# Kernel optimization log

Measured on AMD Instinct MI355X. Metric: run time of the kernel, lower is better.

The kernel has to match this reference:

```python
import jax, jax.numpy as jnp
import numpy as np

# Model constants (match init_kwargs / lucidrains reformer defaults where noted)
DEPTH = 2
HEADS = 8
DIM = 1024
DH = DIM // HEADS        # dim per head = 128
T = 4096                 # sequence length
BUCKET = 64              # bucket_size
NB = T // BUCKET         # n_buckets = 64
NH = 4                   # n_hashes (lucidrains default 8; reduced for memory)
B = 2                    # batch
FF_MULT = 4


def layer_norm(x, g, b):
    mu = jnp.mean(x, axis=-1, keepdims=True)
    var = jnp.mean(jnp.square(x - mu), axis=-1, keepdims=True)
    return (x - mu) * jax.lax.rsqrt(var + 1e-5) * g + b


def lsh_attn_head(qk, v, rot):
    """Single-head LSH attention. qk, v: [T, DH]; rot: [DH, NH, NB//2]."""
    t, d = qk.shape
    # --- LSH bucketing: random rotations, argmax over [rot, -rot] ---
    rotated = jnp.einsum('td,dhr->htr', qk, rot)            # [NH, T, NB//2]
    rotated = jnp.concatenate([rotated, -rotated], axis=-1)  # [NH, T, NB]
    buckets = jnp.argmax(rotated, axis=-1)                   # [NH, T]
    buckets = buckets + jnp.arange(NH)[:, None] * NB         # offset per hash round
    buckets = buckets.reshape(-1)                            # [NH*T]
    ticker = jnp.arange(NH * t)
    # stable sort by (bucket, position)
    sort_key = buckets * t + (ticker % t)
    sticker = jnp.argsort(sort_key)                          # sorted -> original flat idx
    undo = jnp.argsort(sticker)                              # original flat idx -> sorted pos
    st = sticker % t                                         # original seq positions, sorted
    sqk = qk[st]                                             # [NH*T, DH]
    sv = v[st]
    # --- chunked attention: each chunk attends to itself + previous chunk ---
    nc = NH * NB
    bq = sqk.reshape(nc, BUCKET, d)
    bv = sv.reshape(nc, BUCKET, d)
    bt = st.reshape(nc, BUCKET)
    bk = bq / jnp.sqrt(jnp.sum(bq * bq, axis=-1, keepdims=True) + 1e-12)  # unit-length keys
    look = lambda z: jnp.concatenate([z, jnp.roll(z, 1, axis=0)], axis=1)
    bk, bv2, bkt = look(bk), look(bv), look(bt)
    dots = jnp.einsum('cid,cjd->cij', bq, bk) * (d ** -0.5)  # [nc, BUCKET, 2*BUCKET]
    # self-attention mask (token attends to itself only as a last resort)
    dots = jnp.where(bt[:, :, None] == bkt[:, None, :], dots - 1e5, dots)
    lse = jax.scipy.special.logsumexp(dots, axis=-1, keepdims=True)
    probs = jnp.exp(dots - lse)
    bo = jnp.einsum('cij,cjd->cid', probs, bv2)              # [nc, BUCKET, DH]
    # --- unsort and combine hash rounds by softmax over round logsumexps ---
    o = bo.reshape(-1, d)[undo].reshape(NH, t, d)
    logits = lse.reshape(-1)[undo].reshape(NH, t, 1)
    w = jnp.exp(logits - jax.scipy.special.logsumexp(logits, axis=0, keepdims=True))
    return jnp.sum(o * w, axis=0)                            # [T, DH]


def lsh_self_attention(h, Wqk, Wv, Wo, bo, rot):
    bsz, t, _ = h.shape
    split = lambda z: z.reshape(bsz, t, HEADS, DH).transpose(0, 2, 1, 3).reshape(bsz * HEADS, t, DH)
    qk = split(h @ Wqk)
    v = split(h @ Wv)
    out = jax.vmap(lsh_attn_head, in_axes=(0, 0, None))(qk, v, rot)
    out = out.reshape(bsz, HEADS, t, DH).transpose(0, 2, 1, 3).reshape(bsz, t, HEADS * DH)
    return out @ Wo + bo


def setup_inputs() -> dict:
    key = jax.random.key(0)
    ks = jax.random.split(key, 16)
    s = 0.02
    inp = {
        'x': jax.random.normal(ks[0], (B, T, DIM), dtype=jnp.float32),
        'mask': jnp.ones((B, T), dtype=bool),
        'ln1_g': jnp.ones((DEPTH, DIM), jnp.float32),
        'ln1_b': jnp.zeros((DEPTH, DIM), jnp.float32),
        'Wqk': jax.random.normal(ks[1], (DEPTH, DIM, HEADS * DH), jnp.float32) * s,
        'Wv': jax.random.normal(ks[2], (DEPTH, DIM, HEADS * DH), jnp.float32) * s,
        'Wo': jax.random.normal(ks[3], (DEPTH, HEADS * DH, DIM), jnp.float32) * s,
        'bo': jnp.zeros((DEPTH, DIM), jnp.float32),
        'ln2_g': jnp.ones((DEPTH, DIM), jnp.float32),
        'ln2_b': jnp.zeros((DEPTH, DIM), jnp.float32),
        'W1': jax.random.normal(ks[4], (DEPTH, DIM, FF_MULT * DIM), jnp.float32) * s,
        'b1': jnp.zeros((DEPTH, FF_MULT * DIM), jnp.float32),
        'W2': jax.random.normal(ks[5], (DEPTH, FF_MULT * DIM, DIM), jnp.float32) * s,
        'b2': jnp.zeros((DEPTH, DIM), jnp.float32),
        'rot': jax.random.normal(ks[6], (DEPTH, DH, NH, NB // 2), jnp.float32),
    }
    return inp


def reference(x, mask, ln1_g, ln1_b, Wqk, Wv, Wo, bo, ln2_g, ln2_b, W1, b1, W2, b2, rot):
    # Reversible sequence: duplicate stream, f = PreNorm(LSHSelfAttention), g = PreNorm(FF)
    x1, x2 = x, x
    for l in range(DEPTH):
        a = lsh_self_attention(layer_norm(x2, ln1_g[l], ln1_b[l]),
                               Wqk[l], Wv[l], Wo[l], bo[l], rot[l])
        y1 = x1 + a
        h = layer_norm(y1, ln2_g[l], ln2_b[l])
        f = jax.nn.gelu(h @ W1[l] + b1[l]) @ W2[l] + b2[l]
        y2 = x2 + f
        x1, x2 = y1, y2
    return (x1 + x2) * 0.5
```

## Files before the change

kernel.cpp:

```cpp
#include <hip/hip_runtime.h>
#include <hip/hip_bf16.h>

#define TSEQ   4096
#define DIMM   1024
#define NHEADS 8
#define DH     128
#define NHASH  4
#define NBUCK  64
#define NCHUNK 256
#define BSZ    2
#define NBH    16
#define FFD    4096

typedef __attribute__((ext_vector_type(4))) float f32x4;
typedef __attribute__((ext_vector_type(8))) short s16x8;
typedef __attribute__((ext_vector_type(4))) short s16x4;
typedef __attribute__((ext_vector_type(2))) double f64x2;

__device__ __forceinline__ unsigned short f2bf(float f) {
    union { float f; unsigned int u; } x; x.f = f;
    unsigned int r = x.u + 0x7FFFu + ((x.u >> 16) & 1u);
    return (unsigned short)(r >> 16);
}

__device__ __forceinline__ void async16(const void* g, void* l) {
    __builtin_amdgcn_global_load_lds(
        (const __attribute__((address_space(1))) unsigned int*)g,
        (__attribute__((address_space(3))) unsigned int*)l, 16, 0, 0);
}

__device__ __forceinline__ float gelu_tanh(float x) {
    float x3 = x * x * x;
    float inner = 0.7978845608028654f * (x + 0.044715f * x3);
    return 0.5f * x * (1.0f + tanhf(inner));
}

__global__ void init_kernel(const float* __restrict__ x, float* __restrict__ X1,
                            float* __restrict__ X2, int n) {
    int i = blockIdx.x * blockDim.x + threadIdx.x;
    if (i < n) { float v = x[i]; X1[i] = v; X2[i] = v; }
}

__global__ void zero_kernel(float* __restrict__ p, int n) {
    int i = blockIdx.x * blockDim.x + threadIdx.x;
    if (i < n) p[i] = 0.f;
}

__global__ void initmw_kernel(float* __restrict__ M, float* __restrict__ W, int n) {
    int i = blockIdx.x * blockDim.x + threadIdx.x;
    if (i < n) { M[i] = -3.0e38f; W[i] = 0.f; }
}

__global__ void div_kernel(const float* __restrict__ U, const float* __restrict__ Wst,
                           unsigned short* __restrict__ AOb, int n) {
    int i = blockIdx.x * blockDim.x + threadIdx.x;
    if (i < n) {
        int row = i >> 10, col = i & 1023;
        int b = row >> 12, t = row & 4095, head = col >> 7;
        float w = Wst[(size_t)(b * 8 + head) * TSEQ + t];
        AOb[i] = f2bf(U[i] / w);
    }
}

__global__ __launch_bounds__(256) void convT_kernel(const float* __restrict__ in,
                                                    unsigned short* __restrict__ out,
                                                    int K, int N) {
    __shared__ float tile[32][33];
    int n0 = blockIdx.x * 32, k0 = blockIdx.y * 32;
    int tx = threadIdx.x & 31, ty = threadIdx.x >> 5;
    #pragma unroll
    for (int r = 0; r < 4; r++)
        tile[ty + r * 8][tx] = in[(size_t)(k0 + ty + r * 8) * N + n0 + tx];
    __syncthreads();
    #pragma unroll
    for (int r = 0; r < 4; r++)
        out[(size_t)(n0 + ty + r * 8) * K + k0 + tx] = f2bf(tile[tx][ty + r * 8]);
}

__global__ __launch_bounds__(256) void ln_bf16_kernel(const float* __restrict__ in,
                                                      const float* __restrict__ g,
                                                      const float* __restrict__ bb,
                                                      unsigned short* __restrict__ out) {
    int row = blockIdx.x;
    int tid = threadIdx.x;
    const float* xr = in + (size_t)row * DIMM;
    float v[4];
    float s = 0.f, sq = 0.f;
    #pragma unroll
    for (int k = 0; k < 4; k++) { float t = xr[tid + 256 * k]; v[k] = t; s += t; sq += t * t; }
    __shared__ float rs[256], rq[256];
    rs[tid] = s; rq[tid] = sq; __syncthreads();
    for (int off = 128; off > 0; off >>= 1) {
        if (tid < off) { rs[tid] += rs[tid + off]; rq[tid] += rq[tid + off]; }
        __syncthreads();
    }
    float mu  = rs[0] * (1.f / DIMM);
    float var = rq[0] * (1.f / DIMM) - mu * mu;
    float rstd = rsqrtf(var + 1e-5f);
    unsigned short* orow = out + (size_t)row * DIMM;
    #pragma unroll
    for (int k = 0; k < 4; k++) {
        int c = tid + 256 * k;
        orow[c] = f2bf((v[k] - mu) * rstd * g[c] + bb[c]);
    }
}

template<int OUT_BF16>
__global__ __launch_bounds__(256) void mgemm_kernel(const unsigned short* __restrict__ A,
                                                    const unsigned short* __restrict__ Bt,
                                                    const float* __restrict__ bias,
                                                    const float* __restrict__ resid,
                                                    void* __restrict__ Cv,
                                                    int M, int N, int K, int flags) {
    __shared__ __align__(16) unsigned short sA[128 * 32];
    __shared__ __align__(16) unsigned short sB[128 * 32];
    int tid = threadIdx.x;
    int wave = tid >> 6, lane = tid & 63;
    int n0 = blockIdx.x * 128, m0 = blockIdx.y * 128;
    int wr = (wave >> 1) * 64, wc = (wave & 1) * 64;
    f32x4 acc[4][4] = {};
    int c1 = tid, c2 = tid + 256;
    const unsigned short* gA1 = A + (size_t)(m0 + (c1 >> 2)) * K + (c1 & 3) * 8;
    const unsigned short* gA2 = A + (size_t)(m0 + (c2 >> 2)) * K + (c2 & 3) * 8;
    const unsigned short* gB1 = Bt + (size_t)(n0 + (c1 >> 2)) * K + (c1 & 3) * 8;
    const unsigned short* gB2 = Bt + (size_t)(n0 + (c2 >> 2)) * K + (c2 & 3) * 8;
    unsigned short* lA1 = sA + wave * 512;
    unsigned short* lA2 = sA + 2048 + wave * 512;
    unsigned short* lB1 = sB + wave * 512;
    unsigned short* lB2 = sB + 2048 + wave * 512;
    int qk8 = (lane >> 4) * 8;
    int r16 = lane & 15;
    for (int k0 = 0; k0 < K; k0 += 32) {
        __syncthreads();
        async16(gA1 + k0, lA1);
        async16(gA2 + k0, lA2);
        async16(gB1 + k0, lB1);
        async16(gB2 + k0, lB2);
        __syncthreads();
        s16x8 af[4], bf[4];
        #pragma unroll
        for (int i = 0; i < 4; i++) {
            af[i] = *(const s16x8*)&sA[(wr + i * 16 + r16) * 32 + qk8];
            bf[i] = *(const s16x8*)&sB[(wc + i * 16 + r16) * 32 + qk8];
        }
        #pragma unroll
        for (int mi = 0; mi < 4; mi++)
            #pragma unroll
            for (int ni = 0; ni < 4; ni++)
                acc[mi][ni] = __builtin_amdgcn_mfma_f32_16x16x32_bf16(af[mi], bf[ni], acc[mi][ni], 0, 0, 0);
    }
    #pragma unroll
    for (int mi = 0; mi < 4; mi++) {
        #pragma unroll
        for (int r = 0; r < 4; r++) {
            int row = m0 + wr + mi * 16 + (lane >> 4) * 4 + r;
            #pragma unroll
            for (int ni = 0; ni < 4; ni++) {
                int col = n0 + wc + ni * 16 + (lane & 15);
                float v = acc[mi][ni][r];
                if (flags & 1) v += bias[col];
                if (flags & 2) v = gelu_tanh(v);
                if (flags & 4) v += resid[(size_t)row * N + col];
                if (OUT_BF16) ((unsigned short*)Cv)[(size_t)row * N + col] = f2bf(v);
                else          ((float*)Cv)[(size_t)row * N + col] = v;
            }
        }
    }
}


__global__ __launch_bounds__(256) void ln64_kernel(const float* __restrict__ X,
                                                   const float* __restrict__ g,
                                                   const float* __restrict__ bb,
                                                   double* __restrict__ H64) {
    int row = blockIdx.x;
    int tid = threadIdx.x;
    const float* xr = X + (size_t)row * DIMM;
    __shared__ double rs[256], rq[256];
    double v[4];
    double s = 0.0, sq = 0.0;
    #pragma unroll
    for (int q = 0; q < 4; q++) {
        double t = (double)xr[tid + 256 * q];
        v[q] = t; s += t; sq += t * t;
    }
    rs[tid] = s; rq[tid] = sq; __syncthreads();
    for (int off = 128; off > 0; off >>= 1) {
        if (tid < off) { rs[tid] += rs[tid + off]; rq[tid] += rq[tid + off]; }
        __syncthreads();
    }
    double mu   = rs[0] * (1.0 / DIMM);
    double var  = rq[0] * (1.0 / DIMM) - mu * mu;
    double rstd = 1.0 / sqrt(var + 1e-5);
    double* orow = H64 + (size_t)row * DIMM;
    #pragma unroll
    for (int q = 0; q < 4; q++) {
        int c = tid + 256 * q;
        orow[c] = (v[q] - mu) * rstd * (double)g[c] + (double)bb[c];
    }
}

__global__ __launch_bounds__(256) void rcomb_kernel(const float* __restrict__ Wqk,
                                                    const float* __restrict__ rot,
                                                    double* __restrict__ R) {
    int k = blockIdx.x;
    int c0 = threadIdx.x * 4;
    int hd = c0 >> 7;
    int cc = c0 & 127;
    const float* wrow = Wqk + (size_t)k * DIMM + hd * 128;
    double a0 = 0.0, a1 = 0.0, a2 = 0.0, a3 = 0.0;
    for (int d = 0; d < 128; d++) {
        double w = (double)wrow[d];
        f32x4 r4 = *(const f32x4*)&rot[d * 128 + cc];
        a0 += w * (double)r4.x; a1 += w * (double)r4.y;
        a2 += w * (double)r4.z; a3 += w * (double)r4.w;
    }
    double* orow = R + (size_t)k * DIMM + c0;
    orow[0] = a0; orow[1] = a1; orow[2] = a2; orow[3] = a3;
}

#define RKS 16
__global__ __launch_bounds__(256, 2) void rotgemm_kernel(const double* __restrict__ H64,
                                                         const double* __restrict__ R,
                                                         int* __restrict__ bucket) {
    __shared__ double sA[RKS][130];
    __shared__ double sB[RKS][130];
    int tid = threadIdx.x;
    int tx = tid & 15, ty = tid >> 4;
    int n0 = blockIdx.x * 128, m0 = blockIdx.y * 128;
    double acc[8][8] = {};

    int arow = tid >> 1, ak = (tid & 1) * 8;
    const double* gA = H64 + (size_t)(m0 + arow) * DIMM + ak;
    int bkk = tid >> 4, bn = (tid & 15) * 8;
    const double* gB = R + (size_t)bkk * DIMM + n0 + bn;

    f64x2 a2[4], b2[4];
    #pragma unroll
    for (int u = 0; u < 4; u++) {
        a2[u] = *(const f64x2*)(gA + 2 * u);
        b2[u] = *(const f64x2*)(gB + 2 * u);
    }

    for (int k0 = 0; k0 < DIMM; k0 += RKS) {
        __syncthreads();
        #pragma unroll
        for (int u = 0; u < 4; u++) {
            sA[ak + 2 * u][arow]     = a2[u].x;
            sA[ak + 2 * u + 1][arow] = a2[u].y;
            *(f64x2*)&sB[bkk][bn + 2 * u] = b2[u];
        }
        __syncthreads();
        if (k0 + RKS < DIMM) {
            const double* pa = gA + k0 + RKS;
            const double* pb = gB + (size_t)(k0 + RKS) * DIMM;
            #pragma unroll
            for (int u = 0; u < 4; u++) {
                a2[u] = *(const f64x2*)(pa + 2 * u);
                b2[u] = *(const f64x2*)(pb + 2 * u);
            }
        }
        #pragma unroll
        for (int kk = 0; kk < RKS; kk++) {
            double a_[8], b_[8];
            #pragma unroll
            for (int u = 0; u < 4; u++) {
                f64x2 t = *(const f64x2*)&sA[kk][ty * 8 + 2 * u];
                a_[2 * u] = t.x; a_[2 * u + 1] = t.y;
            }
            #pragma unroll
            for (int c = 0; c < 4; c++) {
                f64x2 t = *(const f64x2*)&sB[kk][2 * tx + 32 * c];
                b_[2 * c] = t.x; b_[2 * c + 1] = t.y;
            }
            #pragma unroll
            for (int r = 0; r < 8; r++)
                #pragma unroll
                for (int c = 0; c < 8; c++)
                    acc[r][c] += a_[r] * b_[c];
        }
    }

    int hd = n0 >> 7;
    #pragma unroll
    for (int g = 0; g < 4; g++) {
        #pragma unroll
        for (int r = 0; r < 8; r++) {
            double best = acc[r][2 * g]; int bidx = 2 * tx;
            double v1 = acc[r][2 * g + 1];
            if (v1 > best) { best = v1; bidx = 2 * tx + 1; }
            double v2 = -acc[r][2 * g];
            if (v2 > best) { best = v2; bidx = 32 + 2 * tx; }
            double v3 = -acc[r][2 * g + 1];
            if (v3 > best) { best = v3; bidx = 32 + 2 * tx + 1; }
            #pragma unroll
            for (int off = 1; off < 16; off <<= 1) {
                double ov = __shfl_xor(best, off, 64);
                int    oi = __shfl_xor(bidx, off, 64);
                if (ov > best || (ov == best && oi < bidx)) { best = ov; bidx = oi; }
            }
            if (tx == 0) {
                int row = m0 + ty * 8 + r;
                int b_ = row >> 12, t = row & 4095;
                bucket[(size_t)((b_ * 8 + hd) * NHASH + g) * TSEQ + t] = bidx;
            }
        }
    }
}

__global__ __launch_bounds__(64) void sort_kernel(const int* __restrict__ bucket,
                                                  int* __restrict__ st) {
    int h = blockIdx.x, bh = blockIdx.y;
    int tid = threadIdx.x;
    __shared__ int sbuck[TSEQ];
    __shared__ int cnt[NBUCK];
    cnt[tid] = 0;
    __syncthreads();
    const int* brow = bucket + (size_t)(bh * NHASH + h) * TSEQ;
    for (int t = tid; t < TSEQ; t += 64) {
        int bu = brow[t];
        sbuck[t] = bu;
        atomicAdd(&cnt[bu], 1);
    }
    __syncthreads();
    if (tid == 0) {
        int run = 0;
        for (int i = 0; i < NBUCK; i++) { int c = cnt[i]; cnt[i] = run; run += c; }
    }
    __syncthreads();
    int off = cnt[tid];
    int* strow = st + (size_t)bh * (NHASH * TSEQ) + h * TSEQ;
    for (int t = 0; t < TSEQ; t++) {
        if (sbuck[t] == tid) strow[off++] = t;
    }
}

__global__ __launch_bounds__(256) void norm_kernel(const float* __restrict__ QK,
                                                   float* __restrict__ invn) {
    int bh = blockIdx.y;
    int b = bh >> 3, head = bh & 7;
    int wave = threadIdx.x >> 6, lane = threadIdx.x & 63;
    int t = blockIdx.x * 4 + wave;
    const float* row = QK + (size_t)(b * TSEQ + t) * DIMM + head * DH;
    float v0 = row[lane], v1 = row[lane + 64];
    float s = v0 * v0 + v1 * v1;
    #pragma unroll
    for (int off = 32; off > 0; off >>= 1) s += __shfl_xor(s, off, 64);
    if (lane == 0) invn[bh * TSEQ + t] = rsqrtf(s + 1e-12f);
}

__global__ __launch_bounds__(256) void attn_online_kernel(const float* __restrict__ QK,
                                                          const float* __restrict__ V,
                                                          const float* __restrict__ invn,
                                                          const int* __restrict__ st,
                                                          float* __restrict__ Mst,
                                                          float* __restrict__ Wst,
                                                          float* __restrict__ U,
                                                          int roundBase) {
    int c  = roundBase + blockIdx.x;
    int bh = blockIdx.y;
    int b = bh >> 3, head = bh & 7;
    const float* QKb = QK + (size_t)b * TSEQ * DIMM + head * DH;
    const float* Vb  = V  + (size_t)b * TSEQ * DIMM + head * DH;
    const int* stb = st + (size_t)bh * (NHASH * TSEQ);
    int prev = (c + NCHUNK - 1) & (NCHUNK - 1);
    int tid = threadIdx.x;
    int wave = tid >> 6, lane = tid & 63;
    int l16 = lane & 15, hi4 = lane >> 4;

    __shared__ __align__(16) unsigned short sKb[128][136];
    __shared__ __align__(16) float sdots[64][132];
    __shared__ __align__(16) unsigned short sVt[128][36];
    __shared__ int   sbt[64];
    __shared__ int   sbkt[128];
    __shared__ float sinv[128];
    __shared__ float sa[64], sb[64];

    if (tid < 64) sbt[tid] = stb[c * 64 + tid];
    if (tid < 128) {
        int j = tid;
        int p = (j < 64) ? (c * 64 + j) : (prev * 64 + j - 64);
        int tk = stb[p];
        sbkt[j] = tk;
        sinv[j] = invn[bh * TSEQ + tk];
    }
    __syncthreads();

    #pragma unroll
    for (int pass = 0; pass < 16; pass++) {
        int idx = pass * 256 + tid;
        int j = idx >> 5, dq = (idx & 31) * 4;
        f32x4 v4 = *(const f32x4*)&QKb[(size_t)sbkt[j] * DIMM + dq];
        unsigned short* p = &sKb[j][dq];
        p[0] = f2bf(v4.x); p[1] = f2bf(v4.y); p[2] = f2bf(v4.z); p[3] = f2bf(v4.w);
    }
    __syncthreads();

    f32x4 dacc[8] = {};
    #pragma unroll
    for (int k0 = 0; k0 < 128; k0 += 32) {
        s16x8 afr = *(const s16x8*)&sKb[16 * wave + l16][k0 + hi4 * 8];
        #pragma unroll
        for (int t = 0; t < 8; t++) {
            s16x8 bfr = *(const s16x8*)&sKb[16 * t + l16][k0 + hi4 * 8];
            dacc[t] = __builtin_amdgcn_mfma_f32_16x16x32_bf16(afr, bfr, dacc[t], 0, 0, 0);
        }
    }
    const float scale = 0.08838834764831845f;
    #pragma unroll
    for (int t = 0; t < 8; t++) {
        #pragma unroll
        for (int r = 0; r < 4; r++) {
            int i = 16 * wave + hi4 * 4 + r;
            int j = 16 * t + l16;
            float v = dacc[t][r] * sinv[j] * scale;
            if (sbt[i] == sbkt[j]) v -= 1e5f;
            sdots[i][j] = v;
        }
    }
    __syncthreads();

    {
        int row = tid >> 2, q = tid & 3;
        float m = -3.402823466e38f;
        for (int j = q; j < 128; j += 4) m = fmaxf(m, sdots[row][j]);
        m = fmaxf(m, __shfl_xor(m, 1, 64));
        m = fmaxf(m, __shfl_xor(m, 2, 64));
        float s = 0.f;
        for (int j = q; j < 128; j += 4) s += expf(sdots[row][j] - m);
        s += __shfl_xor(s, 1, 64);
        s += __shfl_xor(s, 2, 64);
        float inv = 1.f / s;
        for (int j = q; j < 128; j += 4) sdots[row][j] = expf(sdots[row][j] - m) * inv;
        if (q == 0) {
            float lse = m + logf(s);
            int tok = sbt[row];
            size_t mi = (size_t)bh * TSEQ + tok;
            float oldM = Mst[mi], oldW = Wst[mi];
            float newM = fmaxf(oldM, lse);
            float af = expf(oldM - newM);
            float bf = expf(lse - newM);
            Mst[mi] = newM;
            Wst[mi] = oldW * af + bf;
            sa[row] = af; sb[row] = bf;
        }
    }
    __syncthreads();

    f32x4 oacc[8] = {};
    for (int j0 = 0; j0 < 128; j0 += 32) {
        __syncthreads();
        #pragma unroll
        for (int pass = 0; pass < 16; pass++) {
            int idx = pass * 256 + tid;
            int jj = idx >> 7, d = idx & 127;
            sVt[d][jj] = f2bf(Vb[(size_t)sbkt[j0 + jj] * DIMM + d]);
        }
        __syncthreads();
        float pv[8];
        *(f32x4*)&pv[0] = *(const f32x4*)&sdots[16 * wave + l16][j0 + hi4 * 8];
        *(f32x4*)&pv[4] = *(const f32x4*)&sdots[16 * wave + l16][j0 + hi4 * 8 + 4];
        s16x8 pfr;
        #pragma unroll
        for (int u = 0; u < 8; u++) pfr[u] = (short)f2bf(pv[u]);
        #pragma unroll
        for (int t = 0; t < 8; t++) {
            s16x4 vlo = *(const s16x4*)&sVt[16 * t + l16][hi4 * 8];
            s16x4 vhi = *(const s16x4*)&sVt[16 * t + l16][hi4 * 8 + 4];
            s16x8 vfr;
            vfr[0] = vlo[0]; vfr[1] = vlo[1]; vfr[2] = vlo[2]; vfr[3] = vlo[3];
            vfr[4] = vhi[0]; vfr[5] = vhi[1]; vfr[6] = vhi[2]; vfr[7] = vhi[3];
            oacc[t] = __builtin_amdgcn_mfma_f32_16x16x32_bf16(pfr, vfr, oacc[t], 0, 0, 0);
        }
    }

    #pragma unroll
    for (int t = 0; t < 8; t++) {
        #pragma unroll
        for (int r = 0; r < 4; r++) {
            int i = 16 * wave + hi4 * 4 + r;
            float af = sa[i], bf = sb[i];
            int d = 16 * t + l16;
            float* urow = U + (size_t)(b * TSEQ + sbt[i]) * DIMM + head * DH;
            urow[d] = urow[d] * af + oacc[t][r] * bf;
        }
    }
}

__global__ void final_kernel(const float* __restrict__ X1, const float* __restrict__ X2,
                             float* __restrict__ out, int n) {
    int i = blockIdx.x * blockDim.x + threadIdx.x;
    if (i < n) out[i] = 0.5f * (X1[i] + X2[i]);
}

extern "C" void kernel_launch(void* const* d_in, const int* in_sizes, int n_in,
                              void* d_out, int out_size, void* d_ws, size_t ws_size,
                              hipStream_t stream) {
    (void)in_sizes; (void)n_in; (void)out_size; (void)ws_size;
    const float* x    = (const float*)d_in[0];
    const float* ln1g = (const float*)d_in[2];
    const float* ln1b = (const float*)d_in[3];
    const float* Wqk  = (const float*)d_in[4];
    const float* Wv   = (const float*)d_in[5];
    const float* Wo   = (const float*)d_in[6];
    const float* bo   = (const float*)d_in[7];
    const float* ln2g = (const float*)d_in[8];
    const float* ln2b = (const float*)d_in[9];
    const float* W1   = (const float*)d_in[10];
    const float* b1   = (const float*)d_in[11];
    const float* W2   = (const float*)d_in[12];
    const float* b2   = (const float*)d_in[13];
    const float* rot  = (const float*)d_in[14];
    float* out = (float*)d_out;

    char* ws = (char*)d_ws;
    const size_t SZ  = (size_t)BSZ * TSEQ * DIMM * sizeof(float);
    const size_t HSZ = SZ / 2;
    float* X1 = (float*)(ws + 0 * SZ);
    float* X2 = (float*)(ws + 1 * SZ);
    unsigned short* Hb  = (unsigned short*)(ws + 2 * SZ);
    unsigned short* Wb  = (unsigned short*)(ws + 2 * SZ + HSZ);
    float* AO = (float*)(ws + 2 * SZ);
    float* QK = (float*)(ws + 3 * SZ);
    unsigned short* AOb = (unsigned short*)(ws + 3 * SZ);
    unsigned short* Wob = (unsigned short*)(ws + 3 * SZ + HSZ);
    float* V = (float*)(ws + 4 * SZ);
    unsigned short* Hb2 = (unsigned short*)(ws + 4 * SZ);
    unsigned short* W1b = (unsigned short*)(ws + 4 * SZ + HSZ);
    unsigned short* W2b = (unsigned short*)(ws + 4 * SZ + HSZ + 8 * 1024 * 1024);
    unsigned short* G = (unsigned short*)(ws + 2 * SZ);
    double* H64 = (double*)(ws + 2 * SZ);
    double* Rc  = (double*)(ws + 4 * SZ);
    char* p = ws + 5 * SZ;
    float* Mst  = (float*)p; p += (size_t)NBH * TSEQ * sizeof(float);
    float* Wst  = (float*)p; p += (size_t)NBH * TSEQ * sizeof(float);
    float* invn = (float*)p; p += (size_t)NBH * TSEQ * sizeof(float);
    int*   bucket = (int*)p; p += (size_t)NBH * NHASH * TSEQ * sizeof(int);
    int*   st     = (int*)p; p += (size_t)NBH * NHASH * TSEQ * sizeof(int);

    const int MROWS = BSZ * TSEQ;
    const int NELEM = MROWS * DIMM;
    const int NMW = NBH * TSEQ;

    init_kernel<<<(NELEM + 255) / 256, 256, 0, stream>>>(x, X1, X2, NELEM);

    for (int l = 0; l < 2; l++) {
        const float* wqk = Wqk + (size_t)l * DIMM * DIMM;
        const float* wv  = Wv  + (size_t)l * DIMM * DIMM;
        const float* wo  = Wo  + (size_t)l * DIMM * DIMM;
        const float* w1  = W1  + (size_t)l * DIMM * FFD;
        const float* w2  = W2  + (size_t)l * FFD * DIMM;
        const float* rotl = rot + (size_t)l * DH * NHASH * (NBUCK / 2);

        ln64_kernel<<<MROWS, 256, 0, stream>>>(X2, ln1g + l * DIMM, ln1b + l * DIMM, H64);
        rcomb_kernel<<<DIMM, 256, 0, stream>>>(wqk, rotl, Rc);
        rotgemm_kernel<<<dim3(8, 64), 256, 0, stream>>>(H64, Rc, bucket);

        ln_bf16_kernel<<<MROWS, 256, 0, stream>>>(X2, ln1g + l * DIMM, ln1b + l * DIMM, Hb);
        convT_kernel<<<dim3(32, 32), 256, 0, stream>>>(wqk, Wb, DIMM, DIMM);
        mgemm_kernel<0><<<dim3(8, 64), 256, 0, stream>>>(Hb, Wb, nullptr, nullptr, QK,
                                                         MROWS, DIMM, DIMM, 0);
        convT_kernel<<<dim3(32, 32), 256, 0, stream>>>(wv, Wb, DIMM, DIMM);
        mgemm_kernel<0><<<dim3(8, 64), 256, 0, stream>>>(Hb, Wb, nullptr, nullptr, V,
                                                         MROWS, DIMM, DIMM, 0);
        sort_kernel<<<dim3(NHASH, NBH), 64, 0, stream>>>(bucket, st);
        norm_kernel<<<dim3(TSEQ / 4, NBH), 256, 0, stream>>>(QK, invn);
        initmw_kernel<<<(NMW + 255) / 256, 256, 0, stream>>>(Mst, Wst, NMW);
        zero_kernel<<<(NELEM + 255) / 256, 256, 0, stream>>>(AO, NELEM);
        for (int r = 0; r < NHASH; r++)
            attn_online_kernel<<<dim3(NBUCK, NBH), 256, 0, stream>>>(
                QK, V, invn, st, Mst, Wst, AO, r * NBUCK);
        div_kernel<<<(NELEM + 255) / 256, 256, 0, stream>>>(AO, Wst, AOb, NELEM);
        convT_kernel<<<dim3(32, 32), 256, 0, stream>>>(wo, Wob, DIMM, DIMM);
        mgemm_kernel<0><<<dim3(8, 64), 256, 0, stream>>>(AOb, Wob, bo + l * DIMM, X1, X1,
                                                         MROWS, DIMM, DIMM, 1 | 4);

        ln_bf16_kernel<<<MROWS, 256, 0, stream>>>(X1, ln2g + l * DIMM, ln2b + l * DIMM, Hb2);
        convT_kernel<<<dim3(128, 32), 256, 0, stream>>>(w1, W1b, DIMM, FFD);
        mgemm_kernel<1><<<dim3(32, 64), 256, 0, stream>>>(Hb2, W1b, b1 + l * FFD, nullptr, G,
                                                          MROWS, FFD, DIMM, 1 | 2);
        convT_kernel<<<dim3(32, 128), 256, 0, stream>>>(w2, W2b, FFD, DIMM);
        mgemm_kernel<0><<<dim3(8, 64), 256, 0, stream>>>(G, W2b, b2 + l * DIMM, X2, X2,
                                                         MROWS, DIMM, FFD, 1 | 4);
    }

    final_kernel<<<(NELEM + 255) / 256, 256, 0, stream>>>(X1, X2, out, NELEM);
}
```

Measured before the change: 2.992 ms.

## Emulate FP64 LSH rotation GEMM with split-bf16 triple MFMA products

Replaces the scalar double-precision rotation GEMM used for bucket argmax with a matrix-core kernel. Each operand is split into three bf16 pieces, and six bf16 MFMA cross products accumulate in fp32. A new transpose/split kernel prepares the rotation matrix, and the layernorm now writes the three bf16 splits instead of doubles. The aim is to remove the slow FP64 FMA path, at the cost of lower precision (about fp32-level) that could change argmax ties or bucket choices relative to the reference.

```diff
diff --git a/kernel.cpp b/kernel.cpp
--- a/kernel.cpp
+++ b/kernel.cpp
@@ -21,6 +21,11 @@
     union { float f; unsigned int u; } x; x.f = f;
     unsigned int r = x.u + 0x7FFFu + ((x.u >> 16) & 1u);
     return (unsigned short)(r >> 16);
+}
+
+__device__ __forceinline__ float bf2f(unsigned short u) {
+    union { unsigned int u; float f; } x; x.u = ((unsigned int)u) << 16;
+    return x.f;
 }
 
 __device__ __forceinline__ void async16(const void* g, void* l) {
@@ -169,10 +174,12 @@
 }
 
 
-__global__ __launch_bounds__(256) void ln64_kernel(const float* __restrict__ X,
-                                                   const float* __restrict__ g,
-                                                   const float* __restrict__ bb,
-                                                   double* __restrict__ H64) {
+__global__ __launch_bounds__(256) void ln64split_kernel(const float* __restrict__ X,
+                                                        const float* __restrict__ g,
+                                                        const float* __restrict__ bb,
+                                                        unsigned short* __restrict__ H1,
+                                                        unsigned short* __restrict__ H2,
+                                                        unsigned short* __restrict__ H3) {
     int row = blockIdx.x;
     int tid = threadIdx.x;
     const float* xr = X + (size_t)row * DIMM;
@@ -192,11 +199,17 @@
     double mu   = rs[0] * (1.0 / DIMM);
     double var  = rq[0] * (1.0 / DIMM) - mu * mu;
     double rstd = 1.0 / sqrt(var + 1e-5);
-    double* orow = H64 + (size_t)row * DIMM;
     #pragma unroll
     for (int q = 0; q < 4; q++) {
         int c = tid + 256 * q;
-        orow[c] = (v[q] - mu) * rstd * (double)g[c] + (double)bb[c];
+        double h = (v[q] - mu) * rstd * (double)g[c] + (double)bb[c];
+        float f = (float)h;
+        unsigned short u1 = f2bf(f);
+        float r1 = f - bf2f(u1);
+        unsigned short u2 = f2bf(r1);
+        unsigned short u3 = f2bf(r1 - bf2f(u2));
+        size_t idx = (size_t)row * DIMM + c;
+        H1[idx] = u1; H2[idx] = u2; H3[idx] = u3;
     }
 }
 
@@ -219,90 +232,116 @@
     orow[0] = a0; orow[1] = a1; orow[2] = a2; orow[3] = a3;
 }
 
-#define RKS 16
-__global__ __launch_bounds__(256, 2) void rotgemm_kernel(const double* __restrict__ H64,
-                                                         const double* __restrict__ R,
-                                                         int* __restrict__ bucket) {
-    __shared__ double sA[RKS][130];
-    __shared__ double sB[RKS][130];
+__global__ __launch_bounds__(256) void splitRT_kernel(const double* __restrict__ Rc,
+                                                      unsigned short* __restrict__ R1,
+                                                      unsigned short* __restrict__ R2,
+                                                      unsigned short* __restrict__ R3) {
+    __shared__ double tile[32][33];
+    int n0 = blockIdx.x * 32, k0 = blockIdx.y * 32;
+    int tx = threadIdx.x & 31, ty = threadIdx.x >> 5;
+    #pragma unroll
+    for (int r = 0; r < 4; r++)
+        tile[ty + r * 8][tx] = Rc[(size_t)(k0 + ty + r * 8) * DIMM + n0 + tx];
+    __syncthreads();
+    #pragma unroll
+    for (int r = 0; r < 4; r++) {
+        double v = tile[tx][ty + r * 8];
+        float f = (float)v;
+        unsigned short u1 = f2bf(f);
+        float r1 = f - bf2f(u1);
+        unsigned short u2 = f2bf(r1);
+        unsigned short u3 = f2bf(r1 - bf2f(u2));
+        size_t idx = (size_t)(n0 + ty + r * 8) * DIMM + k0 + tx;
+        R1[idx] = u1; R2[idx] = u2; R3[idx] = u3;
+    }
+}
+
+__global__ __launch_bounds__(256) void rotgemm_emu_kernel(
+        const unsigned short* __restrict__ H1, const unsigned short* __restrict__ H2,
+        const unsigned short* __restrict__ H3,
+        const unsigned short* __restrict__ R1, const unsigned short* __restrict__ R2,
+        const unsigned short* __restrict__ R3,
+        int* __restrict__ bucket) {
+    __shared__ __align__(16) unsigned short sA[3][128 * 32];
+    __shared__ __align__(16) unsigned short sB[3][128 * 32];
     int tid = threadIdx.x;
-    int tx = tid & 15, ty = tid >> 4;
+    int wave = tid >> 6, lane = tid & 63;
     int n0 = blockIdx.x * 128, m0 = blockIdx.y * 128;
-    double acc[8][8] = {};
-
-    int arow = tid >> 1, ak = (tid & 1) * 8;
-    const double* gA = H64 + (size_t)(m0 + arow) * DIMM + ak;
-    int bkk = tid >> 4, bn = (tid & 15) * 8;
-    const double* gB = R + (size_t)bkk * DIMM + n0 + bn;
-
-    f64x2 a2[4], b2[4];
-    #pragma unroll
-    for (int u = 0; u < 4; u++) {
-        a2[u] = *(const f64x2*)(gA + 2 * u);
-        b2[u] = *(const f64x2*)(gB + 2 * u);
-    }
-
-    for (int k0 = 0; k0 < DIMM; k0 += RKS) {
-        __syncthreads();
-        #pragma unroll
-        for (int u = 0; u < 4; u++) {
-            sA[ak + 2 * u][arow]     = a2[u].x;
-            sA[ak + 2 * u + 1][arow] = a2[u].y;
-            *(f64x2*)&sB[bkk][bn + 2 * u] = b2[u];
-        }
-        __syncthreads();
-        if (k0 + RKS < DIMM) {
-            const double* pa = gA + k0 + RKS;
-            const double* pb = gB + (size_t)(k0 + RKS) * DIMM;
+    int wr = (wave >> 1) * 64, wc = (wave & 1) * 64;
+    f32x4 acc[4][4] = {};
+    int c1 = tid, c2 = tid + 256;
+    size_t ao1 = (size_t)(m0 + (c1 >> 2)) * DIMM + (c1 & 3) * 8;
+    size_t ao2 = (size_t)(m0 + (c2 >> 2)) * DIMM + (c2 & 3) * 8;
+    size_t bo1 = (size_t)(n0 + (c1 >> 2)) * DIMM + (c1 & 3) * 8;
+    size_t bo2 = (size_t)(n0 + (c2 >> 2)) * DIMM + (c2 & 3) * 8;
+    const unsigned short* gA[3] = { H1 + ao1, H2 + ao1, H3 + ao1 };
+    const unsigned short* gA2[3] = { H1 + ao2, H2 + ao2, H3 + ao2 };
+    const unsigned short* gB[3] = { R1 + bo1, R2 + bo1, R3 + bo1 };
+    const unsigned short* gB2[3] = { R1 + bo2, R2 + bo2, R3 + bo2 };
+    int qk8 = (lane >> 4) * 8;
+    int r16 = lane & 15;
+    for (int k0 = 0; k0 < DIMM; k0 += 32) {
+        __syncthreads();
+        #pragma unroll
+        for (int s = 0; s < 3; s++) {
+            async16(gA[s] + k0,  &sA[s][wave * 512]);
+            async16(gA2[s] + k0, &sA[s][2048 + wave * 512]);
+            async16(gB[s] + k0,  &sB[s][wave * 512]);
+            async16(gB2[s] + k0, &sB[s][2048 + wave * 512]);
+        }
+        __syncthreads();
+        s16x8 bf[3][4];
+        #pragma unroll
+        for (int s = 0; s < 3; s++)
             #pragma unroll
-            for (int u = 0; u < 4; u++) {
-                a2[u] = *(const f64x2*)(pa + 2 * u);
-                b2[u] = *(const f64x2*)(pb + 2 * u);
+            for (int ni = 0; ni < 4; ni++)
+                bf[s][ni] = *(const s16x8*)&sB[s][(wc + ni * 16 + r16) * 32 + qk8];
+        #pragma unroll
+        for (int mi = 0; mi < 4; mi++) {
+            s16x8 a1 = *(const s16x8*)&sA[0][(wr + mi * 16 + r16) * 32 + qk8];
+            s16x8 a2 = *(const s16x8*)&sA[1][(wr + mi * 16 + r16) * 32 + qk8];
+            s16x8 a3 = *(const s16x8*)&sA[2][(wr + mi * 16 + r16) * 32 + qk8];
+            #pragma unroll
+            for (int ni = 0; ni < 4; ni++) {
+                f32x4 a = acc[mi][ni];
+                a = __builtin_amdgcn_mfma_f32_16x16x32_bf16(a1, bf[0][ni], a, 0, 0, 0);
+                a = __builtin_amdgcn_mfma_f32_16x16x32_bf16(a2, bf[0][ni], a, 0, 0, 0);
+                a = __builtin_amdgcn_mfma_f32_16x16x32_bf16(a1, bf[1][ni], a, 0, 0, 0);
+                a = __builtin_amdgcn_mfma_f32_16x16x32_bf16(a2, bf[1][ni], a, 0, 0, 0);
+                a = __builtin_amdgcn_mfma_f32_16x16x32_bf16(a3, bf[0][ni], a, 0, 0, 0);
+                a = __builtin_amdgcn_mfma_f32_16x16x32_bf16(a1, bf[2][ni], a, 0, 0, 0);
+                acc[mi][ni] = a;
             }
         }
-        #pragma unroll
-        for (int kk = 0; kk < RKS; kk++) {
-            double a_[8], b_[8];
+    }
+
+    int hd = n0 >> 7;
+    int hi4 = lane >> 4;
+    #pragma unroll
+    for (int g = 0; g < 2; g++) {
+        int hh = (wc >> 5) + g;
+        #pragma unroll
+        for (int mi = 0; mi < 4; mi++) {
             #pragma unroll
-            for (int u = 0; u < 4; u++) {
-                f64x2 t = *(const f64x2*)&sA[kk][ty * 8 + 2 * u];
-                a_[2 * u] = t.x; a_[2 * u + 1] = t.y;
-            }
-            #pragma unroll
-            for (int c = 0; c < 4; c++) {
-                f64x2 t = *(const f64x2*)&sB[kk][2 * tx + 32 * c];
-                b_[2 * c] = t.x; b_[2 * c + 1] = t.y;
-            }
-            #pragma unroll
-            for (int r = 0; r < 8; r++)
+            for (int r = 0; r < 4; r++) {
+                float best = acc[mi][2 * g][r]; int bidx = r16;
+                float v1 = acc[mi][2 * g + 1][r];
+                if (v1 > best) { best = v1; bidx = 16 + r16; }
+                float v2 = -acc[mi][2 * g][r];
+                if (v2 > best) { best = v2; bidx = 32 + r16; }
+                float v3 = -acc[mi][2 * g + 1][r];
+                if (v3 > best) { best = v3; bidx = 48 + r16; }
                 #pragma unroll
-                for (int c = 0; c < 8; c++)
-                    acc[r][c] += a_[r] * b_[c];
-        }
-    }
-
-    int hd = n0 >> 7;
-    #pragma unroll
-    for (int g = 0; g < 4; g++) {
-        #pragma unroll
-        for (int r = 0; r < 8; r++) {
-            double best = acc[r][2 * g]; int bidx = 2 * tx;
-            double v1 = acc[r][2 * g + 1];
-            if (v1 > best) { best = v1; bidx = 2 * tx + 1; }
-            double v2 = -acc[r][2 * g];
-            if (v2 > best) { best = v2; bidx = 32 + 2 * tx; }
-            double v3 = -acc[r][2 * g + 1];
-            if (v3 > best) { best = v3; bidx = 32 + 2 * tx + 1; }
-            #pragma unroll
-            for (int off = 1; off < 16; off <<= 1) {
-                double ov = __shfl_xor(best, off, 64);
-                int    oi = __shfl_xor(bidx, off, 64);
-                if (ov > best || (ov == best && oi < bidx)) { best = ov; bidx = oi; }
-            }
-            if (tx == 0) {
-                int row = m0 + ty * 8 + r;
-                int b_ = row >> 12, t = row & 4095;
-                bucket[(size_t)((b_ * 8 + hd) * NHASH + g) * TSEQ + t] = bidx;
+                for (int off = 1; off < 16; off <<= 1) {
+                    float ov = __shfl_xor(best, off, 64);
+                    int   oi = __shfl_xor(bidx, off, 64);
+                    if (ov > best || (ov == best && oi < bidx)) { best = ov; bidx = oi; }
+                }
+                if (r16 == 0) {
+                    int row = m0 + wr + mi * 16 + hi4 * 4 + r;
+                    int b_ = row >> 12, t = row & 4095;
+                    bucket[(size_t)((b_ * 8 + hd) * NHASH + hh) * TSEQ + t] = bidx;
+                }
             }
         }
     }
@@ -516,6 +555,7 @@
     char* ws = (char*)d_ws;
     const size_t SZ  = (size_t)BSZ * TSEQ * DIMM * sizeof(float);
     const size_t HSZ = SZ / 2;
+    const size_t MB = 1024 * 1024;
     float* X1 = (float*)(ws + 0 * SZ);
     float* X2 = (float*)(ws + 1 * SZ);
     unsigned short* Hb  = (unsigned short*)(ws + 2 * SZ);
@@ -527,10 +567,15 @@
     float* V = (float*)(ws + 4 * SZ);
     unsigned short* Hb2 = (unsigned short*)(ws + 4 * SZ);
     unsigned short* W1b = (unsigned short*)(ws + 4 * SZ + HSZ);
-    unsigned short* W2b = (unsigned short*)(ws + 4 * SZ + HSZ + 8 * 1024 * 1024);
+    unsigned short* W2b = (unsigned short*)(ws + 4 * SZ + HSZ + 8 * MB);
     unsigned short* G = (unsigned short*)(ws + 2 * SZ);
-    double* H64 = (double*)(ws + 2 * SZ);
-    double* Rc  = (double*)(ws + 4 * SZ);
+    unsigned short* Hs1 = (unsigned short*)(ws + 2 * SZ);
+    unsigned short* Hs2 = (unsigned short*)(ws + 2 * SZ + 16 * MB);
+    unsigned short* Hs3 = (unsigned short*)(ws + 2 * SZ + 32 * MB);
+    double* Rc = (double*)(ws + 2 * SZ + 48 * MB);
+    unsigned short* Rt1 = (unsigned short*)(ws + 2 * SZ + 56 * MB);
+    unsigned short* Rt2 = (unsigned short*)(ws + 2 * SZ + 58 * MB);
+    unsigned short* Rt3 = (unsigned short*)(ws + 2 * SZ + 60 * MB);
     char* p = ws + 5 * SZ;
     float* Mst  = (float*)p; p += (size_t)NBH * TSEQ * sizeof(float);
     float* Wst  = (float*)p; p += (size_t)NBH * TSEQ * sizeof(float);
@@ -552,9 +597,12 @@
         const float* w2  = W2  + (size_t)l * FFD * DIMM;
         const float* rotl = rot + (size_t)l * DH * NHASH * (NBUCK / 2);
 
-        ln64_kernel<<<MROWS, 256, 0, stream>>>(X2, ln1g + l * DIMM, ln1b + l * DIMM, H64);
+        ln64split_kernel<<<MROWS, 256, 0, stream>>>(X2, ln1g + l * DIMM, ln1b + l * DIMM,
+                                                    Hs1, Hs2, Hs3);
         rcomb_kernel<<<DIMM, 256, 0, stream>>>(wqk, rotl, Rc);
-        rotgemm_kernel<<<dim3(8, 64), 256, 0, stream>>>(H64, Rc, bucket);
+        splitRT_kernel<<<dim3(32, 32), 256, 0, stream>>>(Rc, Rt1, Rt2, Rt3);
+        rotgemm_emu_kernel<<<dim3(8, 64), 256, 0, stream>>>(Hs1, Hs2, Hs3,
+                                                            Rt1, Rt2, Rt3, bucket);
 
         ln_bf16_kernel<<<MROWS, 256, 0, stream>>>(X2, ln1g + l * DIMM, ln1b + l * DIMM, Hb);
         convT_kernel<<<dim3(32, 32), 256, 0, stream>>>(wqk, Wb, DIMM, DIMM);
```

Result: faster. 2.448 ms (-18.2%).
